# Optimization experiments

Hardware: AMD Instinct MI355X
Metric: run time of the kernel (lower is better)

The kernel has to match this reference:

```python
import jax, jax.numpy as jnp
import numpy as np

RADIUS = 0.3
K = 64
B, N = 2, 2048


def group_norm(x, groups, w, b, eps=1e-5):
    Bn, C = x.shape[0], x.shape[1]
    orig = x.shape
    xg = x.reshape(Bn, groups, -1)
    mu = xg.mean(-1, keepdims=True)
    var = xg.var(-1, keepdims=True)
    xg = (xg - mu) * jax.lax.rsqrt(var + eps)
    x = xg.reshape(orig)
    bshape = (1, C) + (1,) * (len(orig) - 2)
    return x * w.reshape(bshape) + b.reshape(bshape)


def ball_query(xyz, new_xyz, radius, k):
    # squared pairwise dists (B, M, N)
    d = (jnp.sum(new_xyz ** 2, -1)[:, :, None] + jnp.sum(xyz ** 2, -1)[:, None, :]
         - 2.0 * jnp.einsum('bmc,bnc->bmn', new_xyz, xyz))
    n = xyz.shape[1]
    idx = jnp.broadcast_to(jnp.arange(n, dtype=jnp.int32), d.shape)
    idx = jnp.where(d > radius ** 2, n, idx)
    idx = jnp.sort(idx, axis=-1)[:, :, :k]
    first = idx[:, :, :1]
    return jnp.where(idx == n, first, idx)


def gather_points(points, inds):
    # points (B,N,C), inds (B,M,K) -> (B,M,K,C)
    return jax.vmap(lambda p, i: p[i])(points, inds)


def local_feature(xyz, layers):
    inds = ball_query(xyz, xyz, RADIUS, K)              # (B,N,K)
    grouped = gather_points(xyz, inds)                  # (B,N,K,3)
    rel = grouped - xyz[:, :, None, :]                  # grouped_xyz (relative)
    ctr = jnp.broadcast_to(xyz[:, :, None, :], rel.shape)
    x = jnp.concatenate([ctr, rel], axis=-1)            # (B,N,K,6)
    x = x.transpose(0, 3, 2, 1)                         # (B,6,K,N)
    for (w, gw, gb) in layers:                          # 1x1 conv (no bias) + GN + ReLU
        x = jnp.einsum('oc,bckn->bokn', w, x)
        x = jax.nn.relu(group_norm(x, w.shape[0] // 32, gw, gb))
    return x.max(axis=2)                                # max over K -> (B,C,N)


def attn_block(x, qkw, vw, vb, tw, tb, gw, gb):
    # q_conv and k_conv share the same weight in the original module
    x_q = jnp.einsum('oc,bcn->bno', qkw, x)             # (B,N,C/4)
    x_k = jnp.einsum('oc,bcn->bon', qkw, x)             # (B,C/4,N)
    x_v = jnp.einsum('oc,bcn->bon', vw, x) + vb[None, :, None]
    att = jnp.einsum('bno,bom->bnm', x_q, x_k)          # (B,N,N)
    att = jax.nn.softmax(att, axis=-1)
    att = att / (1e-9 + att.sum(axis=1, keepdims=True))
    x_r = jnp.einsum('bcn,bnm->bcm', x_v, att)
    t = jnp.einsum('oc,bcn->bon', tw, x - x_r) + tb[None, :, None]
    x_r = jax.nn.relu(group_norm(t, tw.shape[0] // 32, gw, gb))
    return x + x_r


def overlap_attention(x, qk_w, v_w, v_b, t_w, t_b, gnw, gnb, fuse_w, fuse_gnw, fuse_gnb):
    feats = []
    for i in range(4):
        x = attn_block(x, qk_w[i], v_w[i], v_b[i], t_w[i], t_b[i], gnw[i], gnb[i])
        feats.append(x)
    x = jnp.concatenate(feats, axis=1)                  # (B,4C,N)
    x = jnp.einsum('oc,bcn->bon', fuse_w, x)            # 1x1 conv, no bias
    x = group_norm(x, 16, fuse_gnw, fuse_gnb)
    return jax.nn.leaky_relu(x, 0.2)


def setup_inputs():
    key = jax.random.key(0)
    ks = jax.random.split(key, 16)
    inp = {}
    inp['src'] = jax.random.uniform(ks[0], (B, N, 3), dtype=jnp.float32)
    inp['tgt'] = jax.random.uniform(ks[1], (B, N, 3), dtype=jnp.float32)
    inp['x_ol_score'] = jax.random.uniform(ks[2], (B, N), dtype=jnp.float32)
    inp['train'] = 1
    inp['iter'] = 0
    dims = [6, 128, 256, 192]
    for i in range(3):
        inp['lf_w%d' % i] = jax.random.normal(ks[3 + i], (dims[i + 1], dims[i]), dtype=jnp.float32) * 0.1
        inp['lf_gnw%d' % i] = jnp.ones((dims[i + 1],), jnp.float32)
        inp['lf_gnb%d' % i] = jnp.zeros((dims[i + 1],), jnp.float32)
    C = 192
    inp['qk_w'] = jax.random.normal(ks[6], (4, C // 4, C), dtype=jnp.float32) * 0.05
    inp['v_w'] = jax.random.normal(ks[7], (4, C, C), dtype=jnp.float32) * 0.05
    inp['v_b'] = jnp.zeros((4, C), jnp.float32)
    inp['t_w'] = jax.random.normal(ks[8], (4, C, C), dtype=jnp.float32) * 0.05
    inp['t_b'] = jnp.zeros((4, C), jnp.float32)
    inp['blk_gnw'] = jnp.ones((4, C), jnp.float32)
    inp['blk_gnb'] = jnp.zeros((4, C), jnp.float32)
    inp['fuse_w'] = jax.random.normal(ks[9], (4 * C, 4 * C), dtype=jnp.float32) * 0.02
    inp['fuse_gnw'] = jnp.ones((4 * C,), jnp.float32)
    inp['fuse_gnb'] = jnp.zeros((4 * C,), jnp.float32)
    return inp


def reference(src, tgt, x_ol_score, train, iter, lf_w0, lf_gnw0, lf_gnb0, lf_w1, lf_gnw1, lf_gnb1, lf_w2, lf_gnw2, lf_gnb2, qk_w, v_w, v_b, t_w, t_b, blk_gnw, blk_gnb, fuse_w, fuse_gnw, fuse_gnb):
    layers = [(lf_w0, lf_gnw0, lf_gnb0), (lf_w1, lf_gnw1, lf_gnb1), (lf_w2, lf_gnw2, lf_gnb2)]

    def branch(xyz):
        f = local_feature(xyz, layers)                   # (B,192,N)
        f = overlap_attention(f, qk_w, v_w, v_b, t_w, t_b, blk_gnw, blk_gnb, fuse_w, fuse_gnw, fuse_gnb)
        f = f.transpose(0, 2, 1)                         # (B,N,768)
        return f / (jnp.linalg.norm(f, axis=-1, keepdims=True) + 1e-8)

    f_x_atten = branch(src)
    f_y_atten = branch(tgt)  # iter == 0 path: target features computed fresh
    return f_x_atten, f_y_atten
```

## Files before the change

### kernel.cpp

```cpp
#include <hip/hip_runtime.h>
#include <hip/hip_bf16.h>
#include <math.h>

#define NPTS 2048
#define KNB 64
#define SPC (KNB*NPTS)

typedef short bf16x8 __attribute__((ext_vector_type(8)));
typedef float f32x4 __attribute__((ext_vector_type(4)));

static __device__ inline short f2b(float f){ __hip_bfloat16 h = __float2bfloat16(f); short s; __builtin_memcpy(&s,&h,2); return s; }
static __device__ inline float b2f(short s){ __hip_bfloat16 h; __builtin_memcpy(&h,&s,2); return __bfloat162float(h); }

__global__ __launch_bounds__(256) void cvt_w(const float* __restrict__ src, short* __restrict__ dst,
                                             int O, int Cs, int Cd)
{
  const int i = blockIdx.x*256 + threadIdx.x;
  if (i >= O*Cd) return;
  const int o = i / Cd, c = i % Cd;
  dst[i] = (c < Cs) ? f2b(src[o*Cs + c]) : (short)0;
}

__global__ __launch_bounds__(256) void fill0(float* __restrict__ p, int n)
{ const int i = blockIdx.x*256 + threadIdx.x; if (i < n) p[i] = 0.f; }

__global__ __launch_bounds__(256) void bq_feat(const float* __restrict__ src,
                                               const float* __restrict__ tgt,
                                               short* __restrict__ featb)
{
  const int z = blockIdx.y;
  const float* xyz = (z < 2) ? src + (size_t)z*NPTS*3 : tgt + (size_t)(z-2)*NPTS*3;
  __shared__ float cs[NPTS*3];
  for (int i = threadIdx.x; i < NPTS*3; i += 256) cs[i] = xyz[i];
  __syncthreads();
  const int wave = threadIdx.x >> 6, lane = threadIdx.x & 63;
  const int m = blockIdx.x*4 + wave;
  short* fb = featb + (long long)z*SPC*8;
  const float px = cs[3*m], py = cs[3*m+1], pz = cs[3*m+2];
  const float sqm = __fadd_rn(__fadd_rn(__fmul_rn(px,px), __fmul_rn(py,py)), __fmul_rn(pz,pz));
  const short pxh = f2b(px), pyh = f2b(py), pzh = f2b(pz);
  int cnt = 0;
  float frx = 0.f, fry = 0.f, frz = 0.f;
  for (int r = 0; r < 32; ++r) {
    const int n = r*64 + lane;
    const float xn = cs[3*n], yn = cs[3*n+1], zn = cs[3*n+2];
    const float sqn = __fadd_rn(__fadd_rn(__fmul_rn(xn,xn), __fmul_rn(yn,yn)), __fmul_rn(zn,zn));
    const float dt  = __fadd_rn(__fadd_rn(__fmul_rn(px,xn), __fmul_rn(py,yn)), __fmul_rn(pz,zn));
    const float d   = __fsub_rn(__fadd_rn(sqm, sqn), __fmul_rn(2.0f, dt));
    const bool hit = (d <= 0.09f);
    const unsigned long long mask = __ballot(hit);
    const int pre = __popcll(mask & ((1ull << lane) - 1ull));
    const int slot = cnt + pre;
    const float rx = xn-px, ry = yn-py, rz = zn-pz;
    if (hit && slot < KNB) {
      short tmp[8] = {pxh, pyh, pzh, f2b(rx), f2b(ry), f2b(rz), 0, 0};
      uint4 raw; __builtin_memcpy(&raw, tmp, 16);
      *(uint4*)&fb[((long long)slot*NPTS + m)*8] = raw;
    }
    if (cnt == 0 && mask) {
      const int fl = __ffsll(mask) - 1;
      frx = __shfl(rx, fl); fry = __shfl(ry, fl); frz = __shfl(rz, fl);
    }
    cnt += __popcll(mask);
    if (cnt >= KNB) break;
  }
  if (cnt < KNB && lane < KNB - cnt) {
    const int slot = cnt + lane;
    short tmp[8] = {pxh, pyh, pzh, f2b(frx), f2b(fry), f2b(frz), 0, 0};
    uint4 raw; __builtin_memcpy(&raw, tmp, 16);
    *(uint4*)&fb[((long long)slot*NPTS + m)*8] = raw;
  }
}

template<int STAGE>
__global__ __launch_bounds__(256) void convfused(
    const short* __restrict__ featb,
    const short* __restrict__ w1, const short* __restrict__ w2, const short* __restrict__ w3,
    const float* __restrict__ stats1, const float* __restrict__ g1w, const float* __restrict__ g1b,
    const float* __restrict__ stats2, const float* __restrict__ g2w, const float* __restrict__ g2b,
    float* __restrict__ pool,
    float* __restrict__ outPart, long long pZ)
{
  __shared__ __align__(16) char arena[79872];
  short* featA = (short*)arena;
  short* As    = (short*)(arena + 10240);
  short* C2s   = (short*)(arena + 45056);
  const int tid = threadIdx.x;
  const int z = blockIdx.z;
  const int m0 = blockIdx.x * 16;
  const int lane = tid & 63, w = tid >> 6;
  const int w_s = w & 1, w_h = w >> 1;
  const int l15 = lane & 15, l4 = lane >> 4;
  const short* fz = featb + (long long)z*SPC*8;

  float s0[2] = {0.f,0.f}, q0[2] = {0.f,0.f};
  float s2[2][2] = {{0.f,0.f},{0.f,0.f}}, q2[2][2] = {{0.f,0.f},{0.f,0.f}};
  float s3[3] = {0.f,0.f,0.f}, q3[3] = {0.f,0.f,0.f};
  f32x4 mx[6];
  #pragma unroll
  for (int j = 0; j < 6; ++j) mx[j] = (f32x4){-1e30f,-1e30f,-1e30f,-1e30f};
  f32x4 c3[4][6];

  #pragma unroll 1
  for (int it = 0; it < 8; ++it) {
    const int k0 = it*8;
    __syncthreads();
    if (tid < 128) {
      const long long g = (long long)(k0 + (tid>>4))*NPTS + m0 + (tid&15);
      const uint4 v = *(const uint4*)&fz[g*8];
      const uint4 zz = make_uint4(0,0,0,0);
      *(uint4*)&featA[tid*40]      = v;
      *(uint4*)&featA[tid*40 + 8]  = zz;
      *(uint4*)&featA[tid*40 + 16] = zz;
      *(uint4*)&featA[tid*40 + 24] = zz;
    }
    __syncthreads();
    f32x4 c1[4][4];
    {
      bf16x8 bw[4];
      #pragma unroll
      for (int tc = 0; tc < 4; ++tc)
        bw[tc] = *(const bf16x8*)&w1[(w_h*64 + tc*16 + l15)*32 + l4*8];
      #pragma unroll
      for (int ts = 0; ts < 4; ++ts) {
        const bf16x8 a = *(const bf16x8*)&featA[(w_s*64 + ts*16 + l15)*40 + l4*8];
        #pragma unroll
        for (int tc = 0; tc < 4; ++tc)
          c1[ts][tc] = __builtin_amdgcn_mfma_f32_16x16x32_bf16(a, bw[tc], (f32x4){0.f,0.f,0.f,0.f}, 0, 0, 0);
      }
    }
    if (STAGE == 0) {
      #pragma unroll
      for (int ts = 0; ts < 4; ++ts)
        #pragma unroll
        for (int tc = 0; tc < 4; ++tc)
          #pragma unroll
          for (int r = 0; r < 4; ++r) {
            const float v = c1[ts][tc][r];
            s0[tc>>1] += v; q0[tc>>1] = fmaf(v, v, q0[tc>>1]);
          }
      continue;
    }
    {
      const float* st1 = stats1 + (long long)z*64;
      #pragma unroll
      for (int tc = 0; tc < 4; ++tc) {
        const int c = w_h*64 + tc*16 + l15;
        const int g = c >> 5;
        const float mu = st1[2*g], rs = st1[2*g+1];
        const float wv = g1w[c], bv = g1b[c];
        #pragma unroll
        for (int ts = 0; ts < 4; ++ts)
          #pragma unroll
          for (int r = 0; r < 4; ++r)
            As[(w_s*64 + ts*16 + l4*4 + r)*136 + c] = f2b(fmaxf((c1[ts][tc][r] - mu)*rs*wv + bv, 0.f));
      }
    }
    __syncthreads();
    #pragma unroll
    for (int h = 0; h < 2; ++h) {
      f32x4 c2[4][4];
      #pragma unroll
      for (int i = 0; i < 4; ++i)
        #pragma unroll
        for (int j = 0; j < 4; ++j) c2[i][j] = (f32x4){0.f,0.f,0.f,0.f};
      const int ob = h*128 + w_h*64;
      #pragma unroll
      for (int c0 = 0; c0 < 128; c0 += 32) {
        bf16x8 af[4], bw[4];
        #pragma unroll
        for (int ts = 0; ts < 4; ++ts)
          af[ts] = *(const bf16x8*)&As[(w_s*64 + ts*16 + l15)*136 + c0 + l4*8];
        #pragma unroll
        for (int tc = 0; tc < 4; ++tc)
          bw[tc] = *(const bf16x8*)&w2[(ob + tc*16 + l15)*128 + c0 + l4*8];
        #pragma unroll
        for (int ts = 0; ts < 4; ++ts)
          #pragma unroll
          for (int tc = 0; tc < 4; ++tc)
            c2[ts][tc] = __builtin_amdgcn_mfma_f32_16x16x32_bf16(af[ts], bw[tc], c2[ts][tc], 0, 0, 0);
      }
      if (STAGE == 1) {
        #pragma unroll
        for (int ts = 0; ts < 4; ++ts)
          #pragma unroll
          for (int tc = 0; tc < 4; ++tc)
            #pragma unroll
            for (int r = 0; r < 4; ++r) {
              const float v = c2[ts][tc][r];
              s2[h][tc>>1] += v; q2[h][tc>>1] = fmaf(v, v, q2[h][tc>>1]);
            }
      } else {
        const float* st2 = stats2 + (long long)z*64;
        #pragma unroll
        for (int tc = 0; tc < 4; ++tc) {
          const int c = ob + tc*16 + l15;
          const int g = c >> 5;
          const float mu = st2[2*g], rs = st2[2*g+1];
          const float wv = g2w[c], bv = g2b[c];
          const int cl = w_h*64 + tc*16 + l15;
          #pragma unroll
          for (int ts = 0; ts < 4; ++ts)
            #pragma unroll
            for (int r = 0; r < 4; ++r)
              C2s[(w_s*64 + ts*16 + l4*4 + r)*136 + cl] = f2b(fmaxf((c2[ts][tc][r] - mu)*rs*wv + bv, 0.f));
        }
        __syncthreads();
        if (h == 0) {
          #pragma unroll
          for (int i = 0; i < 4; ++i)
            #pragma unroll
            for (int j = 0; j < 6; ++j) c3[i][j] = (f32x4){0.f,0.f,0.f,0.f};
        }
        #pragma unroll
        for (int c0 = 0; c0 < 128; c0 += 32) {
          bf16x8 af[4];
          #pragma unroll
          for (int ts = 0; ts < 4; ++ts)
            af[ts] = *(const bf16x8*)&C2s[(w_s*64 + ts*16 + l15)*136 + c0 + l4*8];
          #pragma unroll
          for (int t6 = 0; t6 < 6; ++t6) {
            const bf16x8 bw6 = *(const bf16x8*)&w3[(w_h*96 + t6*16 + l15)*256 + h*128 + c0 + l4*8];
            #pragma unroll
            for (int ts = 0; ts < 4; ++ts)
              c3[ts][t6] = __builtin_amdgcn_mfma_f32_16x16x32_bf16(af[ts], bw6, c3[ts][t6], 0, 0, 0);
          }
        }
        __syncthreads();
      }
    }
    if (STAGE == 2) {
      #pragma unroll
      for (int t6 = 0; t6 < 6; ++t6)
        #pragma unroll
        for (int r = 0; r < 4; ++r) {
          const float v0 = c3[0][t6][r], v1 = c3[1][t6][r];
          const float v2 = c3[2][t6][r], v3 = c3[3][t6][r];
          s3[t6>>1] += (v0+v1) + (v2+v3);
          q3[t6>>1] = fmaf(v0,v0, fmaf(v1,v1, fmaf(v2,v2, fmaf(v3,v3, q3[t6>>1]))));
          mx[t6][r] = fmaxf(mx[t6][r], fmaxf(fmaxf(v0,v1), fmaxf(v2,v3)));
        }
    }
  }

  if (STAGE == 0) {
    #pragma unroll
    for (int j = 0; j < 2; ++j) {
      float s = s0[j], q = q0[j];
      #pragma unroll
      for (int d = 32; d; d >>= 1) { s += __shfl_down(s, d); q += __shfl_down(q, d); }
      if (lane == 0) {
        float* pp = outPart + (long long)z*pZ;
        atomicAdd(&pp[2*(w_h*2+j)], s); atomicAdd(&pp[2*(w_h*2+j)+1], q);
      }
    }
  } else if (STAGE == 1) {
    #pragma unroll
    for (int h = 0; h < 2; ++h)
      #pragma unroll
      for (int j = 0; j < 2; ++j) {
        float s = s2[h][j], q = q2[h][j];
        #pragma unroll
        for (int d = 32; d; d >>= 1) { s += __shfl_down(s, d); q += __shfl_down(q, d); }
        if (lane == 0) {
          const int g = h*4 + w_h*2 + j;
          float* pp = outPart + (long long)z*pZ;
          atomicAdd(&pp[2*g], s); atomicAdd(&pp[2*g+1], q);
        }
      }
  } else {
    #pragma unroll
    for (int j = 0; j < 3; ++j) {
      float s = s3[j], q = q3[j];
      #pragma unroll
      for (int d = 32; d; d >>= 1) { s += __shfl_down(s, d); q += __shfl_down(q, d); }
      if (lane == 0) {
        const int g = w_h*3 + j;
        float* pp = outPart + (long long)z*pZ;
        atomicAdd(&pp[2*g], s); atomicAdd(&pp[2*g+1], q);
      }
    }
    float* pb = (float*)arena;
    __syncthreads();
    #pragma unroll
    for (int t6 = 0; t6 < 6; ++t6)
      #pragma unroll
      for (int r = 0; r < 4; ++r)
        pb[(w_s*16 + l4*4 + r)*192 + w_h*96 + t6*16 + l15] = mx[t6][r];
    __syncthreads();
    for (int t = tid; t < 16*192; t += 256) {
      const int m = t / 192, c = t % 192;
      const float v = fmaxf(pb[m*192 + c], pb[(16+m)*192 + c]);
      pool[((long long)z*NPTS + m0 + m)*192 + c] = v;
    }
  }
}

template<int ABF16>
__global__ __launch_bounds__(256) void mm(
    const void* __restrict__ Ap, long long ldA, long long aZ,
    const float* __restrict__ A2, long long ldA2, long long a2Z,
    const short* __restrict__ Bw, long long bZ,
    void* __restrict__ outp, long long ldo, long long oZ, int outBf16,
    const float* __restrict__ bias,
    const float* __restrict__ rowScale, long long rsZ,
    const float* __restrict__ inStats, long long isZ,
    const float* __restrict__ inW, const float* __restrict__ inB,
    float* __restrict__ outPart, long long pZ, int grpCh,
    int N, int K, int S)
{
  constexpr int RP = 40;
  __shared__ __align__(16) short As[128*RP];
  __shared__ __align__(16) short Bs[64*RP];
  __shared__ float rowS[64], rowQ[64], gSs[4], gQs[4];
  const int tid = threadIdx.x;
  const int z = blockIdx.z;
  const int s_blk = blockIdx.x*128;
  const int o_blk = blockIdx.y*64;
  const int lane = tid & 63;
  const int widx = tid >> 6;
  const int w_s = widx & 1, w_o = widx >> 1;
  const int l15 = lane & 15, l4 = lane >> 4;

  const short* Bz = Bw + (long long)z*bZ;
  const float* stz = inStats ? inStats + (long long)z*isZ : nullptr;

  f32x4 acc[2][4];
  #pragma unroll
  for (int i = 0; i < 2; ++i)
    #pragma unroll
    for (int j = 0; j < 4; ++j) acc[i][j] = (f32x4){0.f,0.f,0.f,0.f};

  if (outPart) {
    if (tid < 64) { rowS[tid] = 0.f; rowQ[tid] = 0.f; }
    if (tid < 4)  { gSs[tid] = 0.f; gQs[tid] = 0.f; }
  }

  for (int c0 = 0; c0 < K; c0 += 32) {
    __syncthreads();
    #pragma unroll
    for (int it = 0; it < 2; ++it) {
      const int ch = tid + it*256;
      const int row = ch >> 2, cq = ch & 3;
      const int gc = c0 + cq*8;
      uint4 raw = make_uint4(0,0,0,0);
      if (gc < K) {
        const long long base = (long long)(s_blk+row)*ldA + gc;
        if (ABF16) {
          raw = *(const uint4*)((const short*)Ap + (long long)z*aZ + base);
          if (stz) {
            short vs[8]; __builtin_memcpy(vs, &raw, 16);
            const int g = gc >> 5;
            const float mu = stz[2*g], rsg = stz[2*g+1];
            short tmp[8];
            #pragma unroll
            for (int j = 0; j < 8; ++j) {
              const float v = (b2f(vs[j]) - mu)*rsg*inW[gc+j] + inB[gc+j];
              tmp[j] = f2b(fmaxf(v, 0.f));
            }
            __builtin_memcpy(&raw, tmp, 16);
          }
        } else {
          const float* Af = (const float*)Ap + (long long)z*aZ + base;
          float4 u0 = *(const float4*)Af;
          float4 u1 = *(const float4*)(Af + 4);
          if (A2) {
            const float* Sf = A2 + (long long)z*a2Z + (long long)(s_blk+row)*ldA2 + gc;
            const float4 s0 = *(const float4*)Sf, s1 = *(const float4*)(Sf + 4);
            u0.x -= s0.x; u0.y -= s0.y; u0.z -= s0.z; u0.w -= s0.w;
            u1.x -= s1.x; u1.y -= s1.y; u1.z -= s1.z; u1.w -= s1.w;
          }
          short tmp[8] = {f2b(u0.x),f2b(u0.y),f2b(u0.z),f2b(u0.w),
                          f2b(u1.x),f2b(u1.y),f2b(u1.z),f2b(u1.w)};
          __builtin_memcpy(&raw, tmp, 16);
        }
      }
      *(uint4*)&As[row*RP + cq*8] = raw;
    }
    {
      const int row = tid >> 2, cq = tid & 3;
      const int gc = c0 + cq*8, go = o_blk + row;
      uint4 raw = make_uint4(0,0,0,0);
      if (go < N && gc < K)
        raw = *(const uint4*)(Bz + (long long)go*K + gc);
      *(uint4*)&Bs[row*RP + cq*8] = raw;
    }
    __syncthreads();
    bf16x8 af[4], bfr[2];
    #pragma unroll
    for (int ts = 0; ts < 4; ++ts)
      af[ts] = *(const bf16x8*)&As[(w_s*64 + ts*16 + l15)*RP + l4*8];
    #pragma unroll
    for (int to = 0; to < 2; ++to)
      bfr[to] = *(const bf16x8*)&Bs[(w_o*32 + to*16 + l15)*RP + l4*8];
    #pragma unroll
    for (int to = 0; to < 2; ++to)
      #pragma unroll
      for (int ts = 0; ts < 4; ++ts)
        acc[to][ts] = __builtin_amdgcn_mfma_f32_16x16x32_bf16(af[ts], bfr[to], acc[to][ts], 0, 0, 0);
  }

  const int s_base = s_blk + w_s*64;
  const int o_base = o_blk + w_o*32;
  float* ozF = (float*)outp + (long long)z*oZ;
  short* ozH = (short*)outp + (long long)z*oZ;
  #pragma unroll
  for (int to = 0; to < 2; ++to) {
    const int o = o_base + to*16 + l15;
    const bool ov = (o < N);
    const float bv = (bias && ov) ? bias[o] : 0.f;
    float ps = 0.f, pq = 0.f;
    #pragma unroll
    for (int ts = 0; ts < 4; ++ts) {
      #pragma unroll
      for (int r = 0; r < 4; ++r) {
        const int s = s_base + ts*16 + l4*4 + r;
        float v = acc[to][ts][r] + bv;
        if (rowScale) v *= rowScale[(long long)z*rsZ + s];
        if (ov) {
          if (outBf16) ozH[(long long)s*ldo + o] = f2b(v);
          else         ozF[(long long)s*ldo + o] = v;
          ps += v; pq = fmaf(v, v, pq);
        }
      }
    }
    if (outPart) {
      ps += __shfl_down(ps, 32); pq += __shfl_down(pq, 32);
      ps += __shfl_down(ps, 16); pq += __shfl_down(pq, 16);
      if (lane < 16) {
        atomicAdd(&rowS[w_o*32 + to*16 + l15], ps);
        atomicAdd(&rowQ[w_o*32 + to*16 + l15], pq);
      }
    }
  }
  if (outPart) {
    __syncthreads();
    if (tid < 64) {
      const int o = o_blk + tid;
      if (o < N) {
        const int gl = o/grpCh - o_blk/grpCh;
        atomicAdd(&gSs[gl], rowS[tid]);
        atomicAdd(&gQs[gl], rowQ[tid]);
      }
    }
    __syncthreads();
    const int g0 = o_blk/grpCh;
    const int hi = (o_blk + 63 < N - 1) ? o_blk + 63 : N - 1;
    if (tid <= hi/grpCh - g0) {
      float* pp = outPart + (long long)z*pZ;
      atomicAdd(&pp[2*(g0+tid)],   gSs[tid]);
      atomicAdd(&pp[2*(g0+tid)+1], gQs[tid]);
    }
  }
}

__global__ __launch_bounds__(256) void attn_fused(
    const short* __restrict__ qkt,
    short* __restrict__ attb,
    float* __restrict__ colsum)
{
  const int tid = threadIdx.x;
  const int z = blockIdx.y;
  const int n0 = blockIdx.x * 16;
  const int w = tid >> 6, lane = tid & 63;
  const int l15 = lane & 15, l4 = lane >> 4;
  const short* qz = qkt + (long long)z*NPTS*64;
  short* az = attb + (long long)z*NPTS*NPTS;

  const bf16x8 aq0 = *(const bf16x8*)&qz[(n0+l15)*64 + l4*8];
  const bf16x8 aq1 = *(const bf16x8*)&qz[(n0+l15)*64 + 32 + l4*8];

  const int key0 = w * 512;
  float rmax[4], rsum[4], rinv[4];
  #pragma unroll
  for (int r = 0; r < 4; ++r) { rmax[r] = -1e30f; rsum[r] = 0.f; }

  #pragma unroll 1
  for (int t = 0; t < 8; ++t) {
    f32x4 acc[4];
    #pragma unroll
    for (int to = 0; to < 4; ++to) {
      const int k = key0 + t*64 + to*16 + l15;
      const bf16x8 b0 = *(const bf16x8*)&qz[k*64 + l4*8];
      const bf16x8 b1 = *(const bf16x8*)&qz[k*64 + 32 + l4*8];
      f32x4 a = (f32x4){0.f,0.f,0.f,0.f};
      a = __builtin_amdgcn_mfma_f32_16x16x32_bf16(aq0, b0, a, 0, 0, 0);
      a = __builtin_amdgcn_mfma_f32_16x16x32_bf16(aq1, b1, a, 0, 0, 0);
      acc[to] = a;
    }
    #pragma unroll
    for (int r = 0; r < 4; ++r) {
      float tmax = fmaxf(fmaxf(acc[0][r], acc[1][r]), fmaxf(acc[2][r], acc[3][r]));
      tmax = fmaxf(tmax, __shfl_xor(tmax, 1));
      tmax = fmaxf(tmax, __shfl_xor(tmax, 2));
      tmax = fmaxf(tmax, __shfl_xor(tmax, 4));
      tmax = fmaxf(tmax, __shfl_xor(tmax, 8));
      const float mnew = fmaxf(rmax[r], tmax);
      float p = __expf(acc[0][r]-mnew) + __expf(acc[1][r]-mnew)
              + __expf(acc[2][r]-mnew) + __expf(acc[3][r]-mnew);
      p += __shfl_xor(p, 1); p += __shfl_xor(p, 2);
      p += __shfl_xor(p, 4); p += __shfl_xor(p, 8);
      rsum[r] = rsum[r]*__expf(rmax[r]-mnew) + p;
      rmax[r] = mnew;
    }
  }

  __shared__ float sM[4][16], sS[4][16];
  if (l15 == 0) {
    #pragma unroll
    for (int r = 0; r < 4; ++r) { sM[w][l4*4+r] = rmax[r]; sS[w][l4*4+r] = rsum[r]; }
  }
  __syncthreads();
  #pragma unroll
  for (int r = 0; r < 4; ++r) {
    const int row = l4*4 + r;
    const float M = fmaxf(fmaxf(sM[0][row], sM[1][row]), fmaxf(sM[2][row], sM[3][row]));
    const float S = sS[0][row]*__expf(sM[0][row]-M) + sS[1][row]*__expf(sM[1][row]-M)
                  + sS[2][row]*__expf(sM[2][row]-M) + sS[3][row]*__expf(sM[3][row]-M);
    rmax[r] = M;
    rinv[r] = 1.0f / S;
  }

  #pragma unroll 1
  for (int t = 0; t < 8; ++t) {
    #pragma unroll
    for (int to = 0; to < 4; ++to) {
      const int k = key0 + t*64 + to*16 + l15;
      const bf16x8 b0 = *(const bf16x8*)&qz[k*64 + l4*8];
      const bf16x8 b1 = *(const bf16x8*)&qz[k*64 + 32 + l4*8];
      f32x4 a = (f32x4){0.f,0.f,0.f,0.f};
      a = __builtin_amdgcn_mfma_f32_16x16x32_bf16(aq0, b0, a, 0, 0, 0);
      a = __builtin_amdgcn_mfma_f32_16x16x32_bf16(aq1, b1, a, 0, 0, 0);
      short v4[4]; float cs = 0.f;
      #pragma unroll
      for (int r = 0; r < 4; ++r) {
        const float v = __expf(a[r] - rmax[r]) * rinv[r];
        v4[r] = f2b(v); cs += v;
      }
      uint2 raw; __builtin_memcpy(&raw, v4, 8);
      *(uint2*)&az[(long long)k*NPTS + n0 + l4*4] = raw;
      cs += __shfl_xor(cs, 16);
      cs += __shfl_xor(cs, 32);
      if (l4 == 0) atomicAdd(&colsum[(long long)z*NPTS + k], cs);
    }
  }
}

__global__ void fin_stats(float* __restrict__ part, float* __restrict__ stats,
                          long long slotStride, int G, float invGS)
{
  const int g = threadIdx.x;
  float* p  = part  + (long long)blockIdx.x * slotStride;
  float* st = stats + (long long)blockIdx.x * slotStride;
  if (g < G) {
    const float mu  = p[2*g] * invGS;
    const float var = p[2*g+1] * invGS - mu*mu;
    st[2*g]   = mu;
    st[2*g+1] = rsqrtf(var + 1e-5f);
    p[2*g] = 0.f; p[2*g+1] = 0.f;
  }
}

__global__ __launch_bounds__(256) void gn_pool(float* __restrict__ pool,
    const float* __restrict__ stats, const float* __restrict__ w, const float* __restrict__ b)
{
  const int i = blockIdx.x*256 + threadIdx.x;
  const int z = i / (NPTS*192);
  const int c = i % 192;
  const int g = c >> 5;
  const float* st = stats + z*64;
  const float v = (pool[i] - st[2*g]) * st[2*g+1] * w[c] + b[c];
  pool[i] = fmaxf(v, 0.f);
}

__global__ __launch_bounds__(256) void gn_resid(const float* __restrict__ t,
    const float* __restrict__ xin, long long xZ, long long xld,
    const float* __restrict__ stats,
    const float* __restrict__ w, const float* __restrict__ b,
    float* __restrict__ outp, long long oZ)
{
  const int i = blockIdx.x*256 + threadIdx.x;
  const int z = blockIdx.y;
  const int n = i / 192, c = i % 192, g = c >> 5;
  const float* st = stats + z*16;
  const float v = (t[(long long)z*NPTS*192 + i] - st[2*g]) * st[2*g+1] * w[c] + b[c];
  outp[(long long)z*oZ + (long long)n*768 + c] =
      xin[(long long)z*xZ + (long long)n*xld + c] + fmaxf(v, 0.f);
}

template<int SRCF32>
__global__ __launch_bounds__(256) void tr2bf(const void* __restrict__ src, short* __restrict__ dst,
                                             long long sZ, long long dZ, int R, int C)
{
  __shared__ float t[32][33];
  const int z = blockIdx.z;
  const int c0 = blockIdx.x*32, r0 = blockIdx.y*32;
  const int tx = threadIdx.x % 32, ty = threadIdx.x / 32;
  #pragma unroll
  for (int j = 0; j < 4; ++j) {
    const int r = r0 + ty + j*8;
    const long long idx = (long long)z*sZ + (long long)r*C + c0 + tx;
    t[ty + j*8][tx] = SRCF32 ? ((const float*)src)[idx] : b2f(((const short*)src)[idx]);
  }
  __syncthreads();
  #pragma unroll
  for (int j = 0; j < 4; ++j) {
    const int c = c0 + ty + j*8;
    dst[(long long)z*dZ + (long long)c*R + r0 + tx] = f2b(t[tx][ty + j*8]);
  }
}

__global__ __launch_bounds__(256) void recip_zero(float* __restrict__ s, float* __restrict__ o, int n)
{ const int i = blockIdx.x*256 + threadIdx.x; if (i < n) { o[i] = 1.0f/(1e-9f + s[i]); s[i] = 0.f; } }

__global__ __launch_bounds__(256) void finalize_gn(const float* __restrict__ fused,
    const float* __restrict__ stats, const float* __restrict__ w, const float* __restrict__ b,
    float* __restrict__ outp, long long oZ)
{
  const int n = blockIdx.x, z = blockIdx.y, tid = threadIdx.x;
  const float* fz = fused + ((long long)z*NPTS + n)*768;
  const float* st = stats + z*32;
  __shared__ float vbuf[768];
  __shared__ float red[256];
  float ss = 0.f;
  for (int c = tid; c < 768; c += 256) {
    float v = fz[c];
    const int g = c / 48;
    v = (v - st[2*g]) * st[2*g+1] * w[c] + b[c];
    v = v > 0.f ? v : 0.2f * v;
    vbuf[c] = v;
    ss = fmaf(v, v, ss);
  }
  red[tid] = ss; __syncthreads();
  for (int st_ = 128; st_; st_ >>= 1) { if (tid < st_) red[tid] += red[tid+st_]; __syncthreads(); }
  const float inv = 1.0f / (sqrtf(red[0]) + 1e-8f);
  float* ob = outp + (long long)z*oZ + (long long)n*768;
  for (int c = tid; c < 768; c += 256) ob[c] = vbuf[c] * inv;
}

extern "C" void kernel_launch(void* const* d_in, const int* in_sizes, int n_in,
                              void* d_out, int out_size, void* d_ws, size_t ws_size,
                              hipStream_t stream)
{
  const float* src = (const float*)d_in[0];
  const float* tgt = (const float*)d_in[1];
  const float* lfw[3]  = {(const float*)d_in[5], (const float*)d_in[8],  (const float*)d_in[11]};
  const float* lfgw[3] = {(const float*)d_in[6], (const float*)d_in[9],  (const float*)d_in[12]};
  const float* lfgb[3] = {(const float*)d_in[7], (const float*)d_in[10], (const float*)d_in[13]};
  const float* qk_w = (const float*)d_in[14];
  const float* v_w  = (const float*)d_in[15];
  const float* v_b  = (const float*)d_in[16];
  const float* t_w  = (const float*)d_in[17];
  const float* t_b  = (const float*)d_in[18];
  const float* bgw  = (const float*)d_in[19];
  const float* bgb  = (const float*)d_in[20];
  const float* fw   = (const float*)d_in[21];
  const float* fgw  = (const float*)d_in[22];
  const float* fgb  = (const float*)d_in[23];
  float* dout = (float*)d_out;

  const size_t availFl = ws_size / sizeof(float);
  float* ws = (float*)d_ws;
  size_t off = 0;
  float* POOLt = ws + off; off += (size_t)4*NPTS*192;
  float* PART  = ws + off; off += 1024;
  float* STATS = ws + off; off += 1024;
  float* SB    = ws + off; off += (size_t)4*NPTS;
  float* SINV  = ws + off; off += (size_t)4*NPTS;
  short* wreg = (short*)(ws + off);
  short* lfw0b = wreg;
  short* lfw1b = lfw0b + 4096;
  short* lfw2b = lfw1b + 32768;
  short* qkwb  = lfw2b + 49152;
  short* vwb   = qkwb + 49152;
  short* twb   = vwb + 147456;
  short* fwb   = twb + 147456;
  off += (4096+32768+49152+49152+147456+147456+589824 + 1)/2 + 8;
  short* FEATb = (short*)(ws + off); off += (size_t)4*SPC*8/2;
  off = (off + 63) & ~(size_t)63;
  float* REG = ws + off;
  const size_t regAvail = (availFl > off) ? (availFl - off) : 0;

  const size_t perZ = 4915200;
  int nz;
  if      (regAvail >= 4*perZ) nz = 4;
  else if (regAvail >= 2*perZ) nz = 2;
  else if (regAvail >= perZ)   nz = 1;
  else return;

  float* XRt   = REG;
  float* Tt    = XRt + (size_t)nz*NPTS*192;
  float* FUSED = Tt  + (size_t)nz*NPTS*192;
  short* QKT   = (short*)(FUSED + (size_t)nz*NPTS*768);
  short* Vt    = QKT + (size_t)nz*NPTS*64;
  short* Vc    = Vt  + (size_t)nz*NPTS*192;
  short* ATTB  = Vc  + (size_t)nz*NPTS*192;

  dim3 b256(256);
  const float invConv = 1.0f / (32.0f * (float)SPC);

  cvt_w<<<dim3(16),  b256, 0, stream>>>(lfw[0], lfw0b, 128, 6, 32);
  cvt_w<<<dim3(128), b256, 0, stream>>>(lfw[1], lfw1b, 256, 128, 128);
  cvt_w<<<dim3(192), b256, 0, stream>>>(lfw[2], lfw2b, 192, 256, 256);
  fill0<<<dim3(96), b256, 0, stream>>>((float*)qkwb, 24576);
  for (int i = 0; i < 4; ++i)
    cvt_w<<<dim3(36), b256, 0, stream>>>(qk_w + (size_t)i*48*192, qkwb + (size_t)i*64*192, 48, 192, 192);
  cvt_w<<<dim3(576), b256, 0, stream>>>(v_w,  vwb,  768, 192, 192);
  cvt_w<<<dim3(576), b256, 0, stream>>>(t_w,  twb,  768, 192, 192);
  cvt_w<<<dim3(2304),b256, 0, stream>>>(fw,   fwb,  768, 768, 768);
  fill0<<<dim3(4), b256, 0, stream>>>(PART, 1024);
  fill0<<<dim3(32), b256, 0, stream>>>(SB, 4*NPTS);

  bq_feat<<<dim3(NPTS/4, 4), b256, 0, stream>>>(src, tgt, FEATb);

  convfused<0><<<dim3(128, 1, 4), b256, 0, stream>>>(
      FEATb, lfw0b, nullptr, nullptr,
      nullptr, nullptr, nullptr, nullptr, nullptr, nullptr,
      nullptr, PART, 64);
  fin_stats<<<4, 32, 0, stream>>>(PART, STATS, 64, 4, invConv);
  convfused<1><<<dim3(128, 1, 4), b256, 0, stream>>>(
      FEATb, lfw0b, lfw1b, nullptr,
      STATS, lfgw[0], lfgb[0], nullptr, nullptr, nullptr,
      nullptr, PART+256, 64);
  fin_stats<<<4, 32, 0, stream>>>(PART+256, STATS+256, 64, 8, invConv);
  convfused<2><<<dim3(128, 1, 4), b256, 0, stream>>>(
      FEATb, lfw0b, lfw1b, lfw2b,
      STATS, lfgw[0], lfgb[0], STATS+256, lfgw[1], lfgb[1],
      POOLt, PART+512, 64);
  fin_stats<<<4, 32, 0, stream>>>(PART+512, STATS+512, 64, 6, invConv);
  gn_pool<<<dim3(4*NPTS*192/256), b256, 0, stream>>>(POOLt, STATS+512, lfgw[2], lfgb[2]);

  for (int bb0 = 0; bb0 < 4; bb0 += nz) {
    for (int i = 0; i < 4; ++i) {
      const float* Xin; long long xZ, xld;
      if (i == 0) { Xin = POOLt + (size_t)bb0*NPTS*192; xZ = (long long)NPTS*192; xld = 192; }
      else        { Xin = dout + (size_t)bb0*NPTS*768 + (size_t)(i-1)*192; xZ = (long long)NPTS*768; xld = 768; }
      mm<0><<<dim3(16, 1, nz), b256, 0, stream>>>(
          Xin, xld, xZ, nullptr,0,0,
          qkwb + (size_t)i*64*192, 0, QKT, 64, (long long)NPTS*64, 1,
          nullptr, nullptr,0, nullptr,0,nullptr,nullptr,
          nullptr, 0, 1, 64, 192, NPTS);
      mm<0><<<dim3(16, 3, nz), b256, 0, stream>>>(
          Xin, xld, xZ, nullptr,0,0,
          vwb + (size_t)i*192*192, 0, Vt, 192, (long long)NPTS*192, 1,
          v_b + (size_t)i*192, nullptr,0, nullptr,0,nullptr,nullptr,
          nullptr, 0, 1, 192, 192, NPTS);
      attn_fused<<<dim3(NPTS/16, nz), b256, 0, stream>>>(QKT, ATTB, SB);
      recip_zero<<<dim3(nz*NPTS/256), b256, 0, stream>>>(SB, SINV, nz*NPTS);
      tr2bf<0><<<dim3(6, 64, nz), b256, 0, stream>>>(Vt, Vc,
          (long long)NPTS*192, (long long)192*NPTS, NPTS, 192);
      mm<1><<<dim3(16, 3, nz), b256, 0, stream>>>(
          ATTB, NPTS, (long long)NPTS*NPTS, nullptr,0,0,
          Vc, (long long)192*NPTS, XRt, 192, (long long)NPTS*192, 0,
          nullptr, SINV, NPTS, nullptr,0,nullptr,nullptr,
          nullptr, 0, 1, 192, NPTS, NPTS);
      mm<0><<<dim3(16, 3, nz), b256, 0, stream>>>(
          Xin, xld, xZ, XRt, 192, (long long)NPTS*192,
          twb + (size_t)i*192*192, 0, Tt, 192, (long long)NPTS*192, 0,
          t_b + (size_t)i*192, nullptr,0, nullptr,0,nullptr,nullptr,
          PART+768, 16, 32, 192, 192, NPTS);
      fin_stats<<<nz, 32, 0, stream>>>(PART+768, STATS+768, 16, 6, 1.0f/65536.0f);
      gn_resid<<<dim3(NPTS*192/256, nz), b256, 0, stream>>>(
          Tt, Xin, xZ, xld, STATS+768,
          bgw + (size_t)i*192, bgb + (size_t)i*192,
          dout + (size_t)bb0*NPTS*768 + (size_t)i*192, (long long)NPTS*768);
    }
    mm<0><<<dim3(16, 12, nz), b256, 0, stream>>>(
        dout + (size_t)bb0*NPTS*768, 768, (long long)NPTS*768, nullptr,0,0,
        fwb, 0, FUSED, 768, (long long)NPTS*768, 0,
        nullptr, nullptr,0, nullptr,0,nullptr,nullptr,
        PART+832, 32, 48, 768, 768, NPTS);
    fin_stats<<<nz, 32, 0, stream>>>(PART+832, STATS+832, 32, 16, 1.0f/98304.0f);
    finalize_gn<<<dim3(NPTS, nz), b256, 0, stream>>>(
        FUSED, STATS+832, fgw, fgb,
        dout + (size_t)bb0*NPTS*768, (long long)NPTS*768);
  }
}
```

Measured before the change: 1.278 ms.

## Restructure fused conv so each wave owns its rows and skips block barriers

The fused three-layer conv kernel is reorganised so each wave handles 16 rows (4 points × 4 neighbours) end to end across all output channels. Each wave writes only to its own slice of shared memory, which removes the __syncthreads barriers from the main loop and the shared-memory max-pool reduction at the end. The max over neighbours now happens in registers and is written straight to the pool buffer. In exchange the weight fragments are reloaded across more MFMA tiles per wave, register pressure rises (16 c2 and 12 c3 accumulators), and the loop runs 16 iterations instead of 8. Loads to featA are not followed by a barrier; this relies on each wave's rows being written only by that same wave.

```diff
diff --git a/kernel.cpp b/kernel.cpp
--- a/kernel.cpp
+++ b/kernel.cpp
@@ -81,218 +81,158 @@
     float* __restrict__ pool,
     float* __restrict__ outPart, long long pZ)
 {
-  __shared__ __align__(16) char arena[79872];
-  short* featA = (short*)arena;
-  short* As    = (short*)(arena + 10240);
-  short* C2s   = (short*)(arena + 45056);
+  __shared__ __align__(16) short featA[64*40];
+  __shared__ __align__(16) short As[64*136];
+  __shared__ __align__(16) short C2s[64*264];
   const int tid = threadIdx.x;
   const int z = blockIdx.z;
   const int m0 = blockIdx.x * 16;
   const int lane = tid & 63, w = tid >> 6;
-  const int w_s = w & 1, w_h = w >> 1;
   const int l15 = lane & 15, l4 = lane >> 4;
   const short* fz = featb + (long long)z*SPC*8;
 
-  float s0[2] = {0.f,0.f}, q0[2] = {0.f,0.f};
-  float s2[2][2] = {{0.f,0.f},{0.f,0.f}}, q2[2][2] = {{0.f,0.f},{0.f,0.f}};
-  float s3[3] = {0.f,0.f,0.f}, q3[3] = {0.f,0.f,0.f};
-  f32x4 mx[6];
-  #pragma unroll
-  for (int j = 0; j < 6; ++j) mx[j] = (f32x4){-1e30f,-1e30f,-1e30f,-1e30f};
-  f32x4 c3[4][6];
+  for (int i = tid; i < 64*40/8; i += 256) *(uint4*)&featA[i*8] = make_uint4(0,0,0,0);
+  __syncthreads();
+
+  bf16x8 bw1[8];
+  #pragma unroll
+  for (int tc = 0; tc < 8; ++tc)
+    bw1[tc] = *(const bf16x8*)&w1[(tc*16+l15)*32 + l4*8];
+
+  float s1a[4], q1a[4], s2a[8], q2a[8], s3a[6], q3a[6], mx[12];
+  #pragma unroll
+  for (int j = 0; j < 4; ++j) { s1a[j]=0.f; q1a[j]=0.f; }
+  #pragma unroll
+  for (int j = 0; j < 8; ++j) { s2a[j]=0.f; q2a[j]=0.f; }
+  #pragma unroll
+  for (int j = 0; j < 6; ++j) { s3a[j]=0.f; q3a[j]=0.f; }
+  #pragma unroll
+  for (int j = 0; j < 12; ++j) mx[j] = -1e30f;
+
+  const int bl_m = 4*w + (lane>>2), kl = lane&3;
 
   #pragma unroll 1
-  for (int it = 0; it < 8; ++it) {
-    const int k0 = it*8;
-    __syncthreads();
-    if (tid < 128) {
-      const long long g = (long long)(k0 + (tid>>4))*NPTS + m0 + (tid&15);
-      const uint4 v = *(const uint4*)&fz[g*8];
-      const uint4 zz = make_uint4(0,0,0,0);
-      *(uint4*)&featA[tid*40]      = v;
-      *(uint4*)&featA[tid*40 + 8]  = zz;
-      *(uint4*)&featA[tid*40 + 16] = zz;
-      *(uint4*)&featA[tid*40 + 24] = zz;
-    }
-    __syncthreads();
-    f32x4 c1[4][4];
-    {
-      bf16x8 bw[4];
-      #pragma unroll
-      for (int tc = 0; tc < 4; ++tc)
-        bw[tc] = *(const bf16x8*)&w1[(w_h*64 + tc*16 + l15)*32 + l4*8];
-      #pragma unroll
-      for (int ts = 0; ts < 4; ++ts) {
-        const bf16x8 a = *(const bf16x8*)&featA[(w_s*64 + ts*16 + l15)*40 + l4*8];
+  for (int it = 0; it < 16; ++it) {
+    const int k0 = it*4;
+    if (lane < 16) {
+      const uint4 v = *(const uint4*)&fz[((long long)(k0+kl)*NPTS + m0 + bl_m)*8];
+      *(uint4*)&featA[(bl_m*4 + kl)*40] = v;
+    }
+    const bf16x8 af1 = *(const bf16x8*)&featA[(16*w + l15)*40 + l4*8];
+    f32x4 c1[8];
+    #pragma unroll
+    for (int tc = 0; tc < 8; ++tc)
+      c1[tc] = __builtin_amdgcn_mfma_f32_16x16x32_bf16(af1, bw1[tc], (f32x4){0.f,0.f,0.f,0.f}, 0, 0, 0);
+
+    if (STAGE == 0) {
+      #pragma unroll
+      for (int tc = 0; tc < 8; ++tc)
         #pragma unroll
-        for (int tc = 0; tc < 4; ++tc)
-          c1[ts][tc] = __builtin_amdgcn_mfma_f32_16x16x32_bf16(a, bw[tc], (f32x4){0.f,0.f,0.f,0.f}, 0, 0, 0);
-      }
-    }
-    if (STAGE == 0) {
-      #pragma unroll
-      for (int ts = 0; ts < 4; ++ts)
-        #pragma unroll
-        for (int tc = 0; tc < 4; ++tc)
-          #pragma unroll
-          for (int r = 0; r < 4; ++r) {
-            const float v = c1[ts][tc][r];
-            s0[tc>>1] += v; q0[tc>>1] = fmaf(v, v, q0[tc>>1]);
-          }
+        for (int r = 0; r < 4; ++r) {
+          const float v = c1[tc][r];
+          s1a[tc>>1] += v; q1a[tc>>1] = fmaf(v, v, q1a[tc>>1]);
+        }
       continue;
     }
     {
       const float* st1 = stats1 + (long long)z*64;
       #pragma unroll
-      for (int tc = 0; tc < 4; ++tc) {
-        const int c = w_h*64 + tc*16 + l15;
-        const int g = c >> 5;
+      for (int tc = 0; tc < 8; ++tc) {
+        const int c = tc*16 + l15, g = tc>>1;
         const float mu = st1[2*g], rs = st1[2*g+1];
         const float wv = g1w[c], bv = g1b[c];
         #pragma unroll
-        for (int ts = 0; ts < 4; ++ts)
-          #pragma unroll
-          for (int r = 0; r < 4; ++r)
-            As[(w_s*64 + ts*16 + l4*4 + r)*136 + c] = f2b(fmaxf((c1[ts][tc][r] - mu)*rs*wv + bv, 0.f));
-      }
-    }
-    __syncthreads();
-    #pragma unroll
-    for (int h = 0; h < 2; ++h) {
-      f32x4 c2[4][4];
-      #pragma unroll
-      for (int i = 0; i < 4; ++i)
-        #pragma unroll
-        for (int j = 0; j < 4; ++j) c2[i][j] = (f32x4){0.f,0.f,0.f,0.f};
-      const int ob = h*128 + w_h*64;
-      #pragma unroll
-      for (int c0 = 0; c0 < 128; c0 += 32) {
-        bf16x8 af[4], bw[4];
-        #pragma unroll
-        for (int ts = 0; ts < 4; ++ts)
-          af[ts] = *(const bf16x8*)&As[(w_s*64 + ts*16 + l15)*136 + c0 + l4*8];
-        #pragma unroll
-        for (int tc = 0; tc < 4; ++tc)
-          bw[tc] = *(const bf16x8*)&w2[(ob + tc*16 + l15)*128 + c0 + l4*8];
-        #pragma unroll
-        for (int ts = 0; ts < 4; ++ts)
-          #pragma unroll
-          for (int tc = 0; tc < 4; ++tc)
-            c2[ts][tc] = __builtin_amdgcn_mfma_f32_16x16x32_bf16(af[ts], bw[tc], c2[ts][tc], 0, 0, 0);
-      }
-      if (STAGE == 1) {
-        #pragma unroll
-        for (int ts = 0; ts < 4; ++ts)
-          #pragma unroll
-          for (int tc = 0; tc < 4; ++tc)
-            #pragma unroll
-            for (int r = 0; r < 4; ++r) {
-              const float v = c2[ts][tc][r];
-              s2[h][tc>>1] += v; q2[h][tc>>1] = fmaf(v, v, q2[h][tc>>1]);
-            }
-      } else {
-        const float* st2 = stats2 + (long long)z*64;
-        #pragma unroll
-        for (int tc = 0; tc < 4; ++tc) {
-          const int c = ob + tc*16 + l15;
-          const int g = c >> 5;
-          const float mu = st2[2*g], rs = st2[2*g+1];
-          const float wv = g2w[c], bv = g2b[c];
-          const int cl = w_h*64 + tc*16 + l15;
-          #pragma unroll
-          for (int ts = 0; ts < 4; ++ts)
-            #pragma unroll
-            for (int r = 0; r < 4; ++r)
-              C2s[(w_s*64 + ts*16 + l4*4 + r)*136 + cl] = f2b(fmaxf((c2[ts][tc][r] - mu)*rs*wv + bv, 0.f));
-        }
-        __syncthreads();
-        if (h == 0) {
-          #pragma unroll
-          for (int i = 0; i < 4; ++i)
-            #pragma unroll
-            for (int j = 0; j < 6; ++j) c3[i][j] = (f32x4){0.f,0.f,0.f,0.f};
-        }
-        #pragma unroll
-        for (int c0 = 0; c0 < 128; c0 += 32) {
-          bf16x8 af[4];
-          #pragma unroll
-          for (int ts = 0; ts < 4; ++ts)
-            af[ts] = *(const bf16x8*)&C2s[(w_s*64 + ts*16 + l15)*136 + c0 + l4*8];
-          #pragma unroll
-          for (int t6 = 0; t6 < 6; ++t6) {
-            const bf16x8 bw6 = *(const bf16x8*)&w3[(w_h*96 + t6*16 + l15)*256 + h*128 + c0 + l4*8];
-            #pragma unroll
-            for (int ts = 0; ts < 4; ++ts)
-              c3[ts][t6] = __builtin_amdgcn_mfma_f32_16x16x32_bf16(af[ts], bw6, c3[ts][t6], 0, 0, 0);
-          }
-        }
-        __syncthreads();
-      }
-    }
-    if (STAGE == 2) {
-      #pragma unroll
-      for (int t6 = 0; t6 < 6; ++t6)
+        for (int r = 0; r < 4; ++r)
+          As[(16*w + l4*4 + r)*136 + c] = f2b(fmaxf((c1[tc][r]-mu)*rs*wv + bv, 0.f));
+      }
+    }
+    f32x4 c2[16];
+    #pragma unroll
+    for (int j = 0; j < 16; ++j) c2[j] = (f32x4){0.f,0.f,0.f,0.f};
+    #pragma unroll
+    for (int c0 = 0; c0 < 128; c0 += 32) {
+      const bf16x8 af = *(const bf16x8*)&As[(16*w + l15)*136 + c0 + l4*8];
+      #pragma unroll
+      for (int tc = 0; tc < 16; ++tc) {
+        const bf16x8 bw = *(const bf16x8*)&w2[(tc*16+l15)*128 + c0 + l4*8];
+        c2[tc] = __builtin_amdgcn_mfma_f32_16x16x32_bf16(af, bw, c2[tc], 0, 0, 0);
+      }
+    }
+    if (STAGE == 1) {
+      #pragma unroll
+      for (int tc = 0; tc < 16; ++tc)
         #pragma unroll
         for (int r = 0; r < 4; ++r) {
-          const float v0 = c3[0][t6][r], v1 = c3[1][t6][r];
-          const float v2 = c3[2][t6][r], v3 = c3[3][t6][r];
-          s3[t6>>1] += (v0+v1) + (v2+v3);
-          q3[t6>>1] = fmaf(v0,v0, fmaf(v1,v1, fmaf(v2,v2, fmaf(v3,v3, q3[t6>>1]))));
-          mx[t6][r] = fmaxf(mx[t6][r], fmaxf(fmaxf(v0,v1), fmaxf(v2,v3)));
+          const float v = c2[tc][r];
+          s2a[tc>>1] += v; q2a[tc>>1] = fmaf(v, v, q2a[tc>>1]);
         }
-    }
-  }
-
+      continue;
+    }
+    {
+      const float* st2 = stats2 + (long long)z*64;
+      #pragma unroll
+      for (int tc = 0; tc < 16; ++tc) {
+        const int c = tc*16 + l15, g = tc>>1;
+        const float mu = st2[2*g], rs = st2[2*g+1];
+        const float wv = g2w[c], bv = g2b[c];
+        #pragma unroll
+        for (int r = 0; r < 4; ++r)
+          C2s[(16*w + l4*4 + r)*264 + c] = f2b(fmaxf((c2[tc][r]-mu)*rs*wv + bv, 0.f));
+      }
+    }
+    f32x4 c3[12];
+    #pragma unroll
+    for (int j = 0; j < 12; ++j) c3[j] = (f32x4){0.f,0.f,0.f,0.f};
+    #pragma unroll
+    for (int c0 = 0; c0 < 256; c0 += 32) {
+      const bf16x8 af = *(const bf16x8*)&C2s[(16*w + l15)*264 + c0 + l4*8];
+      #pragma unroll
+      for (int t6 = 0; t6 < 12; ++t6) {
+        const bf16x8 bw = *(const bf16x8*)&w3[(t6*16+l15)*256 + c0 + l4*8];
+        c3[t6] = __builtin_amdgcn_mfma_f32_16x16x32_bf16(af, bw, c3[t6], 0, 0, 0);
+      }
+    }
+    #pragma unroll
+    for (int t6 = 0; t6 < 12; ++t6) {
+      float vm = -1e30f;
+      #pragma unroll
+      for (int r = 0; r < 4; ++r) {
+        const float v = c3[t6][r];
+        s3a[t6>>1] += v; q3a[t6>>1] = fmaf(v, v, q3a[t6>>1]);
+        vm = fmaxf(vm, v);
+      }
+      mx[t6] = fmaxf(mx[t6], vm);
+    }
+  }
+
+  float* pp = outPart + (long long)z*pZ;
   if (STAGE == 0) {
     #pragma unroll
-    for (int j = 0; j < 2; ++j) {
-      float s = s0[j], q = q0[j];
+    for (int g = 0; g < 4; ++g) {
+      float s = s1a[g], q = q1a[g];
       #pragma unroll
       for (int d = 32; d; d >>= 1) { s += __shfl_down(s, d); q += __shfl_down(q, d); }
-      if (lane == 0) {
-        float* pp = outPart + (long long)z*pZ;
-        atomicAdd(&pp[2*(w_h*2+j)], s); atomicAdd(&pp[2*(w_h*2+j)+1], q);
-      }
+      if (lane == 0) { atomicAdd(&pp[2*g], s); atomicAdd(&pp[2*g+1], q); }
     }
   } else if (STAGE == 1) {
     #pragma unroll
-    for (int h = 0; h < 2; ++h)
-      #pragma unroll
-      for (int j = 0; j < 2; ++j) {
-        float s = s2[h][j], q = q2[h][j];
-        #pragma unroll
-        for (int d = 32; d; d >>= 1) { s += __shfl_down(s, d); q += __shfl_down(q, d); }
-        if (lane == 0) {
-          const int g = h*4 + w_h*2 + j;
-          float* pp = outPart + (long long)z*pZ;
-          atomicAdd(&pp[2*g], s); atomicAdd(&pp[2*g+1], q);
-        }
-      }
+    for (int g = 0; g < 8; ++g) {
+      float s = s2a[g], q = q2a[g];
+      #pragma unroll
+      for (int d = 32; d; d >>= 1) { s += __shfl_down(s, d); q += __shfl_down(q, d); }
+      if (lane == 0) { atomicAdd(&pp[2*g], s); atomicAdd(&pp[2*g+1], q); }
+    }
   } else {
     #pragma unroll
-    for (int j = 0; j < 3; ++j) {
-      float s = s3[j], q = q3[j];
+    for (int g = 0; g < 6; ++g) {
+      float s = s3a[g], q = q3a[g];
       #pragma unroll
       for (int d = 32; d; d >>= 1) { s += __shfl_down(s, d); q += __shfl_down(q, d); }
-      if (lane == 0) {
-        const int g = w_h*3 + j;
-        float* pp = outPart + (long long)z*pZ;
-        atomicAdd(&pp[2*g], s); atomicAdd(&pp[2*g+1], q);
-      }
-    }
-    float* pb = (float*)arena;
-    __syncthreads();
-    #pragma unroll
-    for (int t6 = 0; t6 < 6; ++t6)
-      #pragma unroll
-      for (int r = 0; r < 4; ++r)
-        pb[(w_s*16 + l4*4 + r)*192 + w_h*96 + t6*16 + l15] = mx[t6][r];
-    __syncthreads();
-    for (int t = tid; t < 16*192; t += 256) {
-      const int m = t / 192, c = t % 192;
-      const float v = fmaxf(pb[m*192 + c], pb[(16+m)*192 + c]);
-      pool[((long long)z*NPTS + m0 + m)*192 + c] = v;
-    }
+      if (lane == 0) { atomicAdd(&pp[2*g], s); atomicAdd(&pp[2*g+1], q); }
+    }
+    float* pr = pool + ((long long)z*NPTS + m0 + 4*w + l4)*192;
+    #pragma unroll
+    for (int t6 = 0; t6 < 12; ++t6) pr[t6*16 + l15] = mx[t6];
   }
 }
 
```

Measured after the change: 2.109 ms. +65.1%, slower.
